# Performance work log

Measured on AMD Instinct MI355X. Metric: run time of the kernel, lower is better.

## Reference

```python
import jax, jax.numpy as jnp
import numpy as np

EPS = 1e-12  # torch F.normalize default eps


def setup_inputs() -> dict:
    key = jax.random.key(0)
    k1, k2, k3 = jax.random.split(key, 3)
    B, T, S = 128, 512, 256
    emission_trajectory = jax.random.uniform(k1, (B, T, S), dtype=jnp.float32)
    weight = jax.random.normal(k2, (S, S), dtype=jnp.float32)
    initial_state = jax.random.normal(k3, (S,), dtype=jnp.float32)
    return {
        "emission_trajectory": emission_trajectory,
        "weight": weight,
        "initial_state": initial_state,
    }


def reference(emission_trajectory, weight, initial_state):
    B, T, S = emission_trajectory.shape
    # row-stochastic transition matrix (softmax over dim=1)
    transition = jax.nn.softmax(weight, axis=1)  # [S, S]
    # initial belief (training path: softmax of learned logits), broadcast to batch
    next_state0 = jnp.broadcast_to(jax.nn.softmax(initial_state), (B, S))

    emissions_t = jnp.swapaxes(emission_trajectory, 0, 1)  # [T, B, S]

    def step(next_state, emission_k):
        # Bayes update: elementwise likelihood, L1 normalize (torch p=1 normalize)
        unnorm = next_state * emission_k  # [B, S]
        l1 = jnp.sum(jnp.abs(unnorm), axis=1, keepdims=True)
        state = unnorm / jnp.maximum(l1, EPS)
        # predict: small GEMM [B,S] @ [S,S]
        next_state = state @ transition
        return next_state, next_state

    _, traj = jax.lax.scan(step, next_state0, emissions_t)  # traj: [T, B, S]
    return jnp.swapaxes(traj, 0, 1)  # [B, T, S]
```

## Files before the change

kernel.cpp:

```cpp
#include <hip/hip_runtime.h>
#include <stdint.h>

namespace {

constexpr int Tn = 512;
constexpr int Sn = 256;
constexpr float EPS = 1e-12f;

typedef _Float16 f16x8 __attribute__((ext_vector_type(8)));
typedef float    f32x4 __attribute__((ext_vector_type(4)));

__device__ __forceinline__ void wg_barrier_lds() {
    asm volatile("s_waitcnt lgkmcnt(0)" ::: "memory");
    __builtin_amdgcn_s_barrier();
}

__launch_bounds__(512, 2)
__global__ void hmm_kernel(const float* __restrict__ emission,
                           const float* __restrict__ weight,
                           const float* __restrict__ init,
                           float* __restrict__ out)
{
    const int tid  = threadIdx.x;
    const int wv   = tid >> 6;
    const int lane = tid & 63;
    const int g    = lane >> 4;
    const int jj   = lane & 15;
    const int cA   = 32 * wv + jj;
    const int cB   = cA + 16;
    const int c32  = 32 * wv + (lane & 31);
    const int b    = blockIdx.x;

    __shared__ __align__(16) _Float16 wf16[2][Sn];
    __shared__ __align__(16) float    s_m[Sn];
    __shared__ __align__(16) float    s_z[Sn];
    __shared__ __align__(16) float    scr[2][Sn];

    {
        const int j = tid & 255, h = tid >> 8;
        const float* wr = weight + j * Sn + h * 128;
        float m = -3.402823466e38f;
        #pragma unroll
        for (int i = 0; i < 128; i += 4) {
            float4 v = *reinterpret_cast<const float4*>(wr + i);
            m = fmaxf(m, fmaxf(fmaxf(v.x, v.y), fmaxf(v.z, v.w)));
        }
        scr[h][j] = m;
        __syncthreads();
        float mj = fmaxf(scr[0][j], scr[1][j]);
        float z0 = 0.f, z1 = 0.f, z2 = 0.f, z3 = 0.f;
        #pragma unroll
        for (int i = 0; i < 128; i += 4) {
            float4 v = *reinterpret_cast<const float4*>(wr + i);
            z0 += expf(v.x - mj); z1 += expf(v.y - mj);
            z2 += expf(v.z - mj); z3 += expf(v.w - mj);
        }
        __syncthreads();
        scr[h][j] = (z0 + z1) + (z2 + z3);
        __syncthreads();
        if (h == 0) {
            s_m[j] = mj;
            s_z[j] = 1.f / (scr[0][j] + scr[1][j]);
        }
        __syncthreads();
    }

    f16x8 bfA[8], bfB[8];
    #pragma unroll
    for (int ck = 0; ck < 8; ++ck) {
        #pragma unroll
        for (int i = 0; i < 8; ++i) {
            const int k = ck * 32 + g * 8 + i;
            const float* wk = weight + (size_t)k * Sn;
            bfA[ck][i] = (_Float16)(expf(wk[cA] - s_m[k]) * s_z[k]);
            bfB[ck][i] = (_Float16)(expf(wk[cB] - s_m[k]) * s_z[k]);
        }
    }
    const f16x8 ones8 = {(_Float16)1.f, (_Float16)1.f, (_Float16)1.f, (_Float16)1.f,
                         (_Float16)1.f, (_Float16)1.f, (_Float16)1.f, (_Float16)1.f};

    const float* em = emission + (size_t)b * Tn * Sn + c32;
    float*       op = out      + (size_t)b * Tn * Sn + c32;
    {
        float i0 = init[lane], i1 = init[lane + 64],
              i2 = init[lane + 128], i3 = init[lane + 192];
        float mx = fmaxf(fmaxf(i0, i1), fmaxf(i2, i3));
        #pragma unroll
        for (int o = 32; o >= 1; o >>= 1) mx = fmaxf(mx, __shfl_xor(mx, o));
        float zz = expf(i0 - mx) + expf(i1 - mx) + expf(i2 - mx) + expf(i3 - mx);
        #pragma unroll
        for (int o = 32; o >= 1; o >>= 1) zz += __shfl_xor(zz, o);
        float u  = expf(init[c32] - mx) / zz;
        float w0 = u * em[0];
        if (lane >= 32) wf16[0][c32] = (_Float16)w0;
    }
    float enext = em[Sn];
    __syncthreads();

#define MFMA(A, B, D) __builtin_amdgcn_mfma_f32_16x16x32_f16((A), (B), (D), 0, 0, 0)

    #pragma unroll 1
    for (int t = 0; t < Tn; ++t) {
        const int p = t & 1;

        f16x8 af[8];
        #pragma unroll
        for (int ck = 0; ck < 8; ++ck)
            af[ck] = *reinterpret_cast<const f16x8*>(&wf16[p][ck * 32 + g * 8]);

        f32x4 dA0 = {0.f,0.f,0.f,0.f}, dA1 = {0.f,0.f,0.f,0.f};
        f32x4 dB0 = {0.f,0.f,0.f,0.f}, dB1 = {0.f,0.f,0.f,0.f};
        f32x4 dS0 = {0.f,0.f,0.f,0.f}, dS1 = {0.f,0.f,0.f,0.f};
        dA0 = MFMA(af[0], bfA[0], dA0); dB0 = MFMA(af[0], bfB[0], dB0); dS0 = MFMA(af[0], ones8, dS0);
        dA1 = MFMA(af[4], bfA[4], dA1); dB1 = MFMA(af[4], bfB[4], dB1); dS1 = MFMA(af[4], ones8, dS1);
        dA0 = MFMA(af[1], bfA[1], dA0); dB0 = MFMA(af[1], bfB[1], dB0); dS0 = MFMA(af[1], ones8, dS0);
        dA1 = MFMA(af[5], bfA[5], dA1); dB1 = MFMA(af[5], bfB[5], dB1); dS1 = MFMA(af[5], ones8, dS1);
        dA0 = MFMA(af[2], bfA[2], dA0); dB0 = MFMA(af[2], bfB[2], dB0); dS0 = MFMA(af[2], ones8, dS0);
        dA1 = MFMA(af[6], bfA[6], dA1); dB1 = MFMA(af[6], bfB[6], dB1); dS1 = MFMA(af[6], ones8, dS1);
        dA0 = MFMA(af[3], bfA[3], dA0); dB0 = MFMA(af[3], bfB[3], dB0); dS0 = MFMA(af[3], ones8, dS0);
        dA1 = MFMA(af[7], bfA[7], dA1); dB1 = MFMA(af[7], bfB[7], dB1); dS1 = MFMA(af[7], ones8, dS1);

        float y  = ((lane & 16) == 0) ? (dA0[0] + dA1[0]) : (dB0[0] + dB1[0]);
        float l1 = fmaxf(dS0[0] + dS1[0], EPS);

        uint32_t ebits = __float_as_uint(l1) & 0x7f800000u;
        float sigma = __uint_as_float(0x7f000000u - ebits);

        float wn = (y * sigma) * enext;
        if (lane >= 32) wf16[p ^ 1][c32] = (_Float16)wn;

        if (lane < 32) op[(size_t)t * Sn] = y * (1.f / l1);

        const int tp = (t + 2 < Tn) ? (t + 2) : (Tn - 1);
        const float e2 = em[(size_t)tp * Sn];
        enext = e2;

        wg_barrier_lds();
    }

#undef MFMA
}

}

extern "C" void kernel_launch(void* const* d_in, const int* in_sizes, int n_in,
                              void* d_out, int out_size, void* d_ws, size_t ws_size,
                              hipStream_t stream) {
    const float* emission = (const float*)d_in[0];
    const float* weight   = (const float*)d_in[1];
    const float* init     = (const float*)d_in[2];
    float* outp = (float*)d_out;
    const int Bn = in_sizes[0] / (Tn * Sn);

    hipLaunchKernelGGL(hmm_kernel, dim3(Bn), dim3(512), 0, stream,
                       emission, weight, init, outp);
}
```

Baseline: 336.4 us.

## Halve workgroup to four waves, each covering 64 columns with all lanes

The block shrinks from 512 to 256 threads. Each wave now computes four 16-column MFMA tiles of the transition GEMM, and every lane holds a useful output instead of half the lanes idling. The per-step row-sum MFMA is now issued once per wave rather than by eight waves, which cuts redundant matrix work and makes the per-step barrier cheaper. The softmax setup is also simplified to one row per thread, so the LDS scratch reduction is no longer needed. The cost is longer MFMA accumulation chains per wave and more B-fragment registers per thread.

```diff
diff --git a/kernel.cpp b/kernel.cpp
--- a/kernel.cpp
+++ b/kernel.cpp
@@ -15,7 +15,7 @@
     __builtin_amdgcn_s_barrier();
 }
 
-__launch_bounds__(512, 2)
+__launch_bounds__(256, 1)
 __global__ void hmm_kernel(const float* __restrict__ emission,
                            const float* __restrict__ weight,
                            const float* __restrict__ init,
@@ -26,61 +26,51 @@
     const int lane = tid & 63;
     const int g    = lane >> 4;
     const int jj   = lane & 15;
-    const int cA   = 32 * wv + jj;
-    const int cB   = cA + 16;
-    const int c32  = 32 * wv + (lane & 31);
     const int b    = blockIdx.x;
 
     __shared__ __align__(16) _Float16 wf16[2][Sn];
     __shared__ __align__(16) float    s_m[Sn];
     __shared__ __align__(16) float    s_z[Sn];
-    __shared__ __align__(16) float    scr[2][Sn];
 
     {
-        const int j = tid & 255, h = tid >> 8;
-        const float* wr = weight + j * Sn + h * 128;
+        const float* wr = weight + (size_t)tid * Sn;
         float m = -3.402823466e38f;
-        #pragma unroll
-        for (int i = 0; i < 128; i += 4) {
+        #pragma unroll 4
+        for (int i = 0; i < Sn; i += 4) {
             float4 v = *reinterpret_cast<const float4*>(wr + i);
             m = fmaxf(m, fmaxf(fmaxf(v.x, v.y), fmaxf(v.z, v.w)));
         }
-        scr[h][j] = m;
-        __syncthreads();
-        float mj = fmaxf(scr[0][j], scr[1][j]);
         float z0 = 0.f, z1 = 0.f, z2 = 0.f, z3 = 0.f;
-        #pragma unroll
-        for (int i = 0; i < 128; i += 4) {
+        #pragma unroll 4
+        for (int i = 0; i < Sn; i += 4) {
             float4 v = *reinterpret_cast<const float4*>(wr + i);
-            z0 += expf(v.x - mj); z1 += expf(v.y - mj);
-            z2 += expf(v.z - mj); z3 += expf(v.w - mj);
+            z0 += expf(v.x - m); z1 += expf(v.y - m);
+            z2 += expf(v.z - m); z3 += expf(v.w - m);
         }
-        __syncthreads();
-        scr[h][j] = (z0 + z1) + (z2 + z3);
-        __syncthreads();
-        if (h == 0) {
-            s_m[j] = mj;
-            s_z[j] = 1.f / (scr[0][j] + scr[1][j]);
-        }
+        s_m[tid] = m;
+        s_z[tid] = 1.f / ((z0 + z1) + (z2 + z3));
         __syncthreads();
     }
 
-    f16x8 bfA[8], bfB[8];
+    f16x8 bf[4][8];
     #pragma unroll
-    for (int ck = 0; ck < 8; ++ck) {
+    for (int s = 0; s < 4; ++s) {
+        const int col = 64 * wv + 16 * s + jj;
         #pragma unroll
-        for (int i = 0; i < 8; ++i) {
-            const int k = ck * 32 + g * 8 + i;
-            const float* wk = weight + (size_t)k * Sn;
-            bfA[ck][i] = (_Float16)(expf(wk[cA] - s_m[k]) * s_z[k]);
-            bfB[ck][i] = (_Float16)(expf(wk[cB] - s_m[k]) * s_z[k]);
+        for (int ck = 0; ck < 8; ++ck) {
+            #pragma unroll
+            for (int i = 0; i < 8; ++i) {
+                const int k = ck * 32 + g * 8 + i;
+                bf[s][ck][i] =
+                    (_Float16)(expf(weight[(size_t)k * Sn + col] - s_m[k]) * s_z[k]);
+            }
         }
     }
     const f16x8 ones8 = {(_Float16)1.f, (_Float16)1.f, (_Float16)1.f, (_Float16)1.f,
                          (_Float16)1.f, (_Float16)1.f, (_Float16)1.f, (_Float16)1.f};
 
-    const float* em = emission + (size_t)b * Tn * Sn + c32;
-    float*       op = out      + (size_t)b * Tn * Sn + c32;
+    const float* em = emission + (size_t)b * Tn * Sn + tid;
+    float*       op = out      + (size_t)b * Tn * Sn + tid;
     {
         float i0 = init[lane], i1 = init[lane + 64],
               i2 = init[lane + 128], i3 = init[lane + 192];
@@ -90,9 +80,9 @@
         float zz = expf(i0 - mx) + expf(i1 - mx) + expf(i2 - mx) + expf(i3 - mx);
         #pragma unroll
         for (int o = 32; o >= 1; o >>= 1) zz += __shfl_xor(zz, o);
-        float u  = expf(init[c32] - mx) / zz;
+        float u  = expf(init[tid] - mx) / zz;
         float w0 = u * em[0];
-        if (lane >= 32) wf16[0][c32] = (_Float16)w0;
+        wf16[0][tid] = (_Float16)w0;
     }
     float enext = em[Sn];
     __syncthreads();
@@ -103,37 +93,33 @@
     for (int t = 0; t < Tn; ++t) {
         const int p = t & 1;
 
-        f16x8 af[8];
+        f32x4 d0 = {0.f,0.f,0.f,0.f}, d1 = {0.f,0.f,0.f,0.f};
+        f32x4 d2 = {0.f,0.f,0.f,0.f}, d3 = {0.f,0.f,0.f,0.f};
+        f32x4 dS = {0.f,0.f,0.f,0.f};
         #pragma unroll
-        for (int ck = 0; ck < 8; ++ck)
-            af[ck] = *reinterpret_cast<const f16x8*>(&wf16[p][ck * 32 + g * 8]);
+        for (int ck = 0; ck < 8; ++ck) {
+            const f16x8 a =
+                *reinterpret_cast<const f16x8*>(&wf16[p][ck * 32 + g * 8]);
+            d0 = MFMA(a, bf[0][ck], d0);
+            d1 = MFMA(a, bf[1][ck], d1);
+            d2 = MFMA(a, bf[2][ck], d2);
+            d3 = MFMA(a, bf[3][ck], d3);
+            dS = MFMA(a, ones8, dS);
+        }
 
-        f32x4 dA0 = {0.f,0.f,0.f,0.f}, dA1 = {0.f,0.f,0.f,0.f};
-        f32x4 dB0 = {0.f,0.f,0.f,0.f}, dB1 = {0.f,0.f,0.f,0.f};
-        f32x4 dS0 = {0.f,0.f,0.f,0.f}, dS1 = {0.f,0.f,0.f,0.f};
-        dA0 = MFMA(af[0], bfA[0], dA0); dB0 = MFMA(af[0], bfB[0], dB0); dS0 = MFMA(af[0], ones8, dS0);
-        dA1 = MFMA(af[4], bfA[4], dA1); dB1 = MFMA(af[4], bfB[4], dB1); dS1 = MFMA(af[4], ones8, dS1);
-        dA0 = MFMA(af[1], bfA[1], dA0); dB0 = MFMA(af[1], bfB[1], dB0); dS0 = MFMA(af[1], ones8, dS0);
-        dA1 = MFMA(af[5], bfA[5], dA1); dB1 = MFMA(af[5], bfB[5], dB1); dS1 = MFMA(af[5], ones8, dS1);
-        dA0 = MFMA(af[2], bfA[2], dA0); dB0 = MFMA(af[2], bfB[2], dB0); dS0 = MFMA(af[2], ones8, dS0);
-        dA1 = MFMA(af[6], bfA[6], dA1); dB1 = MFMA(af[6], bfB[6], dB1); dS1 = MFMA(af[6], ones8, dS1);
-        dA0 = MFMA(af[3], bfA[3], dA0); dB0 = MFMA(af[3], bfB[3], dB0); dS0 = MFMA(af[3], ones8, dS0);
-        dA1 = MFMA(af[7], bfA[7], dA1); dB1 = MFMA(af[7], bfB[7], dB1); dS1 = MFMA(af[7], ones8, dS1);
-
-        float y  = ((lane & 16) == 0) ? (dA0[0] + dA1[0]) : (dB0[0] + dB1[0]);
-        float l1 = fmaxf(dS0[0] + dS1[0], EPS);
+        float y  = (g == 0) ? d0[0] : (g == 1) ? d1[0] : (g == 2) ? d2[0] : d3[0];
+        float l1 = fmaxf(dS[0], EPS);
 
         uint32_t ebits = __float_as_uint(l1) & 0x7f800000u;
         float sigma = __uint_as_float(0x7f000000u - ebits);
 
         float wn = (y * sigma) * enext;
-        if (lane >= 32) wf16[p ^ 1][c32] = (_Float16)wn;
+        wf16[p ^ 1][tid] = (_Float16)wn;
 
-        if (lane < 32) op[(size_t)t * Sn] = y * (1.f / l1);
+        op[(size_t)t * Sn] = y * (1.f / l1);
 
         const int tp = (t + 2 < Tn) ? (t + 2) : (Tn - 1);
-        const float e2 = em[(size_t)tp * Sn];
-        enext = e2;
+        enext = em[(size_t)tp * Sn];
 
         wg_barrier_lds();
     }
@@ -152,6 +138,6 @@
     float* outp = (float*)d_out;
     const int Bn = in_sizes[0] / (Tn * Sn);
 
-    hipLaunchKernelGGL(hmm_kernel, dim3(Bn), dim3(512), 0, stream,
+    hipLaunchKernelGGL(hmm_kernel, dim3(Bn), dim3(256), 0, stream,
                        emission, weight, init, outp);
 }
```

Result: faster. 296.2 us (-11.9%).
